# Kernel tuning notes

Hardware: AMD Instinct MI355X
Metric: run time of the kernel (lower is better)

Reference implementation:

```python
import jax, jax.numpy as jnp
import numpy as np

N_NODES = 4096
N_EDGES = 131072
IN_DIM = 40
HID = 128
OUT = 128
GAT_H = 2
GAT_C = 64
D_MODEL = 128
N_HEAD = 4
FF_DIM = 2048
N_LAYERS = 2
EPS = 1e-5
NEG_SLOPE = 0.2


def _layer_norm(x, g, b):
    mu = x.mean(-1, keepdims=True)
    var = ((x - mu) ** 2).mean(-1, keepdims=True)
    return (x - mu) / jnp.sqrt(var + EPS) * g + b


def _gat_conv(h, src, dst, W, a_src, a_dst, bias):
    # PyG GATConv, concat=True, eval mode (no dropout). Self loops already in (src, dst).
    N = h.shape[0]
    xw = (h @ W.T).reshape(N, GAT_H, GAT_C)          # [N, H, C]
    al_src = (xw * a_src).sum(-1)                     # [N, H]
    al_dst = (xw * a_dst).sum(-1)                     # [N, H]
    e = jax.nn.leaky_relu(al_src[src] + al_dst[dst], NEG_SLOPE)  # [E, H]
    # segment softmax over incoming edges of each dst node
    m = jax.ops.segment_max(e, dst, num_segments=N)
    ex = jnp.exp(e - m[dst])
    s = jax.ops.segment_sum(ex, dst, num_segments=N)
    alpha = ex / (s[dst] + 1e-16)                     # [E, H]
    out = jax.ops.segment_sum(xw[src] * alpha[..., None], dst, num_segments=N)
    return out.reshape(N, GAT_H * GAT_C) + bias


def _encoder_layer(x, p):
    # post-norm nn.TransformerEncoderLayer, relu FFN, eval mode
    (in_w, in_b, out_w, out_b, ln1_g, ln1_b,
     ff_w1, ff_b1, ff_w2, ff_b2, ln2_g, ln2_b) = p
    S, E = x.shape
    Dh = E // N_HEAD
    qkv = x @ in_w.T + in_b                           # [S, 3E]
    q, k, v = [t.reshape(S, N_HEAD, Dh) for t in jnp.split(qkv, 3, axis=-1)]
    scores = jnp.einsum('shd,thd->hst', q, k) / jnp.asarray(np.sqrt(Dh), x.dtype)
    attn = jax.nn.softmax(scores, axis=-1)            # [H, S, S]
    o = jnp.einsum('hst,thd->shd', attn, v).reshape(S, E) @ out_w.T + out_b
    x = _layer_norm(x + o, ln1_g, ln1_b)
    ff = jax.nn.relu(x @ ff_w1.T + ff_b1) @ ff_w2.T + ff_b2
    return _layer_norm(x + ff, ln2_g, ln2_b)


def _forward(floats, edge_index):
    (x, enc_w1, enc_b1, enc_w2, enc_b2,
     gat_w, gat_asrc, gat_adst, gat_b,
     l0_in_w, l0_in_b, l0_out_w, l0_out_b, l0_ln1_g, l0_ln1_b,
     l0_ff_w1, l0_ff_b1, l0_ff_w2, l0_ff_b2, l0_ln2_g, l0_ln2_b,
     l1_in_w, l1_in_b, l1_out_w, l1_out_b, l1_ln1_g, l1_ln1_b,
     l1_ff_w1, l1_ff_b1, l1_ff_w2, l1_ff_b2, l1_ln2_g, l1_ln2_b) = floats
    N = x.shape[0]
    # encoder MLP
    h = jax.nn.relu(x @ enc_w1.T + enc_b1) @ enc_w2.T + enc_b2
    # add one self loop per node (GATConv add_self_loops semantics)
    loop = jnp.arange(N, dtype=edge_index.dtype)
    src = jnp.concatenate([edge_index[0], loop])
    dst = jnp.concatenate([edge_index[1], loop])
    h = _gat_conv(h, src, dst, gat_w, gat_asrc, gat_adst, gat_b)
    layers = [
        (l0_in_w, l0_in_b, l0_out_w, l0_out_b, l0_ln1_g, l0_ln1_b,
         l0_ff_w1, l0_ff_b1, l0_ff_w2, l0_ff_b2, l0_ln2_g, l0_ln2_b),
        (l1_in_w, l1_in_b, l1_out_w, l1_out_b, l1_ln1_g, l1_ln1_b,
         l1_ff_w1, l1_ff_b1, l1_ff_w2, l1_ff_b2, l1_ln2_g, l1_ln2_b),
    ]
    for p in layers:
        h = _encoder_layer(h, p)
    return h


def setup_inputs() -> dict:
    key = jax.random.key(0)
    ks = jax.random.split(key, 40)
    s = 0.05
    inp = {}
    inp['x'] = jax.random.normal(ks[0], (N_NODES, IN_DIM), dtype=jnp.float32)
    # edges with src != dst (self loops added inside reference)
    src = jax.random.randint(ks[1], (N_EDGES,), 0, N_NODES)
    off = jax.random.randint(ks[2], (N_EDGES,), 1, N_NODES)
    dst = (src + off) % N_NODES
    inp['edge_index'] = jnp.stack([src, dst]).astype(jnp.int64)
    inp['enc_w1'] = jax.random.normal(ks[3], (HID, IN_DIM)) * s
    inp['enc_b1'] = jnp.zeros((HID,), jnp.float32)
    inp['enc_w2'] = jax.random.normal(ks[4], (OUT, HID)) * s
    inp['enc_b2'] = jnp.zeros((OUT,), jnp.float32)
    inp['gat_w'] = jax.random.normal(ks[5], (GAT_H * GAT_C, OUT)) * s
    inp['gat_asrc'] = jax.random.normal(ks[6], (GAT_H, GAT_C)) * s
    inp['gat_adst'] = jax.random.normal(ks[7], (GAT_H, GAT_C)) * s
    inp['gat_b'] = jnp.zeros((GAT_H * GAT_C,), jnp.float32)
    for i in range(N_LAYERS):
        k = jax.random.split(ks[8 + i], 8)
        inp[f'l{i}_in_w'] = jax.random.normal(k[0], (3 * D_MODEL, D_MODEL)) * s
        inp[f'l{i}_in_b'] = jnp.zeros((3 * D_MODEL,), jnp.float32)
        inp[f'l{i}_out_w'] = jax.random.normal(k[1], (D_MODEL, D_MODEL)) * s
        inp[f'l{i}_out_b'] = jnp.zeros((D_MODEL,), jnp.float32)
        inp[f'l{i}_ln1_g'] = jnp.ones((D_MODEL,), jnp.float32)
        inp[f'l{i}_ln1_b'] = jnp.zeros((D_MODEL,), jnp.float32)
        inp[f'l{i}_ff_w1'] = jax.random.normal(k[2], (FF_DIM, D_MODEL)) * s
        inp[f'l{i}_ff_b1'] = jnp.zeros((FF_DIM,), jnp.float32)
        inp[f'l{i}_ff_w2'] = jax.random.normal(k[3], (D_MODEL, FF_DIM)) * s
        inp[f'l{i}_ff_b2'] = jnp.zeros((D_MODEL,), jnp.float32)
        inp[f'l{i}_ln2_g'] = jnp.ones((D_MODEL,), jnp.float32)
        inp[f'l{i}_ln2_b'] = jnp.zeros((D_MODEL,), jnp.float32)
    return inp


def reference(x, edge_index, enc_w1, enc_b1, enc_w2, enc_b2,
              gat_w, gat_asrc, gat_adst, gat_b,
              l0_in_w, l0_in_b, l0_out_w, l0_out_b, l0_ln1_g, l0_ln1_b,
              l0_ff_w1, l0_ff_b1, l0_ff_w2, l0_ff_b2, l0_ln2_g, l0_ln2_b,
              l1_in_w, l1_in_b, l1_out_w, l1_out_b, l1_ln1_g, l1_ln1_b,
              l1_ff_w1, l1_ff_b1, l1_ff_w2, l1_ff_b2, l1_ln2_g, l1_ln2_b):
    floats = (x, enc_w1, enc_b1, enc_w2, enc_b2,
              gat_w, gat_asrc, gat_adst, gat_b,
              l0_in_w, l0_in_b, l0_out_w, l0_out_b, l0_ln1_g, l0_ln1_b,
              l0_ff_w1, l0_ff_b1, l0_ff_w2, l0_ff_b2, l0_ln2_g, l0_ln2_b,
              l1_in_w, l1_in_b, l1_out_w, l1_out_b, l1_ln1_g, l1_ln1_b,
              l1_ff_w1, l1_ff_b1, l1_ff_w2, l1_ff_b2, l1_ln2_g, l1_ln2_b)
    return _forward(floats, edge_index)
```

## Files before the change

kernel.cpp:

```cpp
#include <hip/hip_runtime.h>
#include <hip/hip_bf16.h>

typedef __hip_bfloat16 bf16;

#define N_NODES 4096
#define IN_DIM  40
#define DM      128
#define FF_DIM  2048
#define GAT_H   2
#define GAT_C   64
#define NHEAD   4
#define DH      32
#define LN_EPS  1e-5f
#define KSPLIT  4
#define FSPLIT  4

typedef short s8v __attribute__((ext_vector_type(8)));
typedef float f4v __attribute__((ext_vector_type(4)));

#define WO_ENC1 0
#define WO_ENC2 8192
#define WO_GAT  24576
#define WO_L(L) (40960 + (L) * 589824)
#define WO_IN(L)  (WO_L(L))
#define WO_OUT(L) (WO_L(L) + 49152)
#define WO_FF1(L) (WO_L(L) + 65536)
#define WO_FF2(L) (WO_L(L) + 327680)
#define WBUF_ELEMS 1220608

__device__ __forceinline__ float anyload(const void* p, size_t i, int isbf) {
    if (isbf) return __bfloat162float(((const bf16*)p)[i]);
    return ((const float*)p)[i];
}
__device__ __forceinline__ int geti(const int* ei, int i, int is64) {
    return is64 ? ei[2 * (size_t)i] : ei[i];
}
__device__ __forceinline__ ushort tob(float v) {
    bf16 b = __float2bfloat16(v);
    return *(ushort*)&b;
}

__global__ __launch_bounds__(256) void setup_kernel(const void* ones_vec, const int* ei,
                                                    int* flags, int* __restrict__ deg,
                                                    const void* enc_w1, const void* enc_w2,
                                                    const void* gat_w,
                                                    const void* in_w0, const void* out_w0,
                                                    const void* ff_w10, const void* ff_w20,
                                                    const void* in_w1, const void* out_w1,
                                                    const void* ff_w11, const void* ff_w21,
                                                    ushort* __restrict__ wbuf) {
    const int isbf = (((const unsigned*)ones_vec)[0] == 0x3F803F80u) ? 1 : 0;
    int gid = blockIdx.x * 256 + threadIdx.x;
    if (gid < N_NODES) deg[gid] = 0;
    if (gid == 0) {
        flags[0] = isbf;
        const unsigned* e = (const unsigned*)ei;
        flags[1] = (e[1] == 0u && e[3] == 0u && e[5] == 0u && e[7] == 0u) ? 1 : 0;
    }
    int base = gid * 4;
#pragma unroll
    for (int j = 0; j < 4; ++j) {
        int i = base + j;
        if (i >= WBUF_ELEMS) break;
        if (i < WO_ENC2) {
            int r = i >> 6, c = i & 63;
            float v = (c < IN_DIM) ? anyload(enc_w1, (size_t)r * IN_DIM + c, isbf) : 0.f;
            wbuf[i] = tob(v);
            continue;
        }
        const void* s;
        int si;
        if      (i < WO_GAT)     { s = enc_w2; si = i - WO_ENC2; }
        else if (i < WO_L(0))    { s = gat_w;  si = i - WO_GAT; }
        else if (i < WO_OUT(0))  { s = in_w0;  si = i - WO_IN(0); }
        else if (i < WO_FF1(0))  { s = out_w0; si = i - WO_OUT(0); }
        else if (i < WO_FF2(0))  { s = ff_w10; si = i - WO_FF1(0); }
        else if (i < WO_L(1))    { s = ff_w20; si = i - WO_FF2(0); }
        else if (i < WO_OUT(1))  { s = in_w1;  si = i - WO_IN(1); }
        else if (i < WO_FF1(1))  { s = out_w1; si = i - WO_OUT(1); }
        else if (i < WO_FF2(1))  { s = ff_w11; si = i - WO_FF1(1); }
        else                     { s = ff_w21; si = i - WO_FF2(1); }
        wbuf[i] = isbf ? ((const ushort*)s)[si] : tob(((const float*)s)[si]);
    }
}

#define K128STR 136

__global__ __launch_bounds__(256) void encgat_kernel(const void* __restrict__ X,
                                                     const void* __restrict__ b1v,
                                                     const void* __restrict__ b2v,
// ... 97 lines not shown
#pragma unroll
    for (int nc = 0; nc < 2; ++nc) {
        int cc = w * 32 + nc * 16 + col;
#pragma unroll
        for (int r = 0; r < 4; ++r) {
            int row = quad * 4 + r;
            float v = acc3[nc][r];
            xwout[(size_t)(row0 + row) * DM + cc] = v;
            Cs[row][cc] = v;
        }
    }
    __syncthreads();
#pragma unroll
    for (int rr = 0; rr < 4; ++rr) {
        int row = w * 4 + rr;
        float x0 = Cs[row][lane], x1 = Cs[row][64 + lane];
        float s0 = x0 * anyload(asrc, lane, isbf);
        float d0 = x0 * anyload(adst, lane, isbf);
        float s1 = x1 * anyload(asrc, 64 + lane, isbf);
        float d1 = x1 * anyload(adst, 64 + lane, isbf);
#pragma unroll
        for (int o = 32; o >= 1; o >>= 1) {
            s0 += __shfl_xor(s0, o); d0 += __shfl_xor(d0, o);
            s1 += __shfl_xor(s1, o); d1 += __shfl_xor(d1, o);
        }
        if (lane == 0) {
            int n = row0 + row;
            als[n * 2 + 0] = s0; ald[n * 2 + 0] = d0;
            als[n * 2 + 1] = s1; ald[n * 2 + 1] = d1;
        }
    }
}

__global__ __launch_bounds__(256) void gemm32_kernel(const ushort* __restrict__ A,
                                                     const ushort* __restrict__ Wb,
                                                     const void* __restrict__ bias,
                                                     ushort* __restrict__ Cb,
                                                     ushort* __restrict__ vtb,
                                                     int N,
                                                     const int* __restrict__ flags,
                                                     int relu) {
    const int isbf = flags[0];
    const int t = threadIdx.x;
    const int w = t >> 6, lane = t & 63;
    const int col = lane & 15, quad = lane >> 4;
    const int wr = (w & 1) * 16, wc = (w >> 1) * 32;
    const int row0 = blockIdx.y * 32, col0 = blockIdx.x * 64;
    __shared__ __align__(16) ushort As[32 * K128STR];
    __shared__ __align__(16) ushort Ws[64 * K128STR];
#pragma unroll
    for (int i = 0; i < 2; ++i) {
        int idx = t + i * 256;
        int r = idx >> 4, c = (idx & 15) * 8;
        *(uint4*)&As[r * K128STR + c] = *(const uint4*)&A[(size_t)(row0 + r) * DM + c];
    }
#pragma unroll
    for (int i = 0; i < 4; ++i) {
        int idx = t + i * 256;
        int r = idx >> 4, c = (idx & 15) * 8;
        *(uint4*)&Ws[r * K128STR + c] = *(const uint4*)&Wb[(size_t)(col0 + r) * DM + c];
    }
    __syncthreads();
    f4v zero = {0.f, 0.f, 0.f, 0.f};
    f4v acc[2] = {zero, zero};
#pragma unroll
    for (int j = 0; j < 4; ++j) {
        s8v a = *(const s8v*)&As[(wr + col) * K128STR + j * 32 + quad * 8];
#pragma unroll
        for (int nc = 0; nc < 2; ++nc) {
            s8v b = *(const s8v*)&Ws[(wc + nc * 16 + col) * K128STR + j * 32 + quad * 8];
            acc[nc] = __builtin_amdgcn_mfma_f32_16x16x32_bf16(a, b, acc[nc], 0, 0, 0);
        }
    }
#pragma unroll
    for (int nc = 0; nc < 2; ++nc) {
        int cc = col0 + wc + nc * 16 + col;
        float bv = bias ? anyload(bias, cc, isbf) : 0.f;
#pragma unroll
        for (int r = 0; r < 4; ++r) {
            int rr = row0 + wr + quad * 4 + r;
            float v = acc[nc][r] + bv;
            if (relu) v = fmaxf(v, 0.f);
            Cb[(size_t)rr * N + cc] = tob(v);
            if (vtb && cc >= 256) vtb[(size_t)(cc - 256) * N_NODES + rr] = tob(v);
        }
    }
}

__global__ __launch_bounds__(256) void oproj_ln_kernel(const float* __restrict__ pO,
                                                       const float* __restrict__ pL,
                                                       const ushort* __restrict__ Wb,
                                                       const void* __restrict__ bias,
                                                       float* __restrict__ h,
                                                       ushort* __restrict__ hb,
                                                       const void* __restrict__ g,
                                                       const void* __restrict__ b,
                                                       const int* __restrict__ flags) {
    const int isbf = flags[0];
    const int t = threadIdx.x;
    const int w = t >> 6, lane = t & 63;
    const int col = lane & 15, quad = lane >> 4;
    const int row0 = blockIdx.x * 16;
    __shared__ __align__(16) ushort As[16 * K128STR];
    __shared__ __align__(16) ushort Ws[128 * K128STR];
    __shared__ float Cs[16][132];

    {
        int ar = t >> 4, ac = (t & 15) * 8;
        int rr = row0 + ar;
        int hh = ac >> 5, d0 = ac & 31;
        size_t qi0 = ((size_t)rr) * NHEAD + hh;
        float lsum = 0.f;
        float osum[8] = {};
#pragma unroll
        for (int kz = 0; kz < KSPLIT; ++kz) {
            size_t qi = qi0 + (size_t)kz * N_NODES * NHEAD;
            lsum += pL[qi];
            const float* po = &pO[qi * 32 + d0];
#pragma unroll
            for (int j = 0; j < 8; ++j) osum[j] += po[j];
        }
        float inv = 1.f / lsum;
#pragma unroll
        for (int j = 0; j < 8; ++j) As[ar * K128STR + ac + j] = tob(osum[j] * inv);
    }
#pragma unroll
    for (int i = 0; i < 8; ++i) {
        int idx = t + i * 256;
        int r = idx >> 4, c = (idx & 15) * 8;
        *(uint4*)&Ws[r * K128STR + c] = *(const uint4*)&Wb[(size_t)r * DM + c];
    }
    __syncthreads();
    f4v zero = {0.f, 0.f, 0.f, 0.f};
    f4v acc[2] = {zero, zero};
#pragma unroll
    for (int j = 0; j < 4; ++j) {
        s8v a = *(const s8v*)&As[col * K128STR + j * 32 + quad * 8];
#pragma unroll
        for (int nc = 0; nc < 2; ++nc) {
            s8v b = *(const s8v*)&Ws[(w * 32 + nc * 16 + col) * K128STR + j * 32 + quad * 8];
            acc[nc] = __builtin_amdgcn_mfma_f32_16x16x32_bf16(a, b, acc[nc], 0, 0, 0);
        }
    }
#pragma unroll
    for (int nc = 0; nc < 2; ++nc) {
        int cc = w * 32 + nc * 16 + col;
        float bv = bias ? anyload(bias, cc, isbf) : 0.f;
#pragma unroll
        for (int r = 0; r < 4; ++r)
            Cs[quad * 4 + r][cc] = acc[nc][r] + bv;
    }
    __syncthreads();
#pragma unroll
    for (int rr = 0; rr < 4; ++rr) {
        int row = w * 4 + rr;
        size_t base = (size_t)(row0 + row) * DM;
        float v0 = h[base + lane] + Cs[row][lane];
        float v1 = h[base + 64 + lane] + Cs[row][64 + lane];
        float s = v0 + v1;
#pragma unroll
        for (int o = 32; o >= 1; o >>= 1) s += __shfl_xor(s, o);
        float mu = s * (1.f / DM);
        float d0 = v0 - mu, d1 = v1 - mu;
        float q = d0 * d0 + d1 * d1;
#pragma unroll
        for (int o = 32; o >= 1; o >>= 1) q += __shfl_xor(q, o);
        float rstd = rsqrtf(q * (1.f / DM) + LN_EPS);
        float o0 = d0 * rstd * anyload(g, lane, isbf) + anyload(b, lane, isbf);
        float o1 = d1 * rstd * anyload(g, 64 + lane, isbf) + anyload(b, 64 + lane, isbf);
        h[base + lane] = o0;       h[base + 64 + lane] = o1;
        hb[base + lane] = tob(o0); hb[base + 64 + lane] = tob(o1);
    }
}

__global__ __launch_bounds__(256) void ff2_splitk_kernel(const ushort* __restrict__ A,
                                                         const ushort* __restrict__ Wb,
                                                         float* __restrict__ Cpart) {
    const int t = threadIdx.x;
    const int w = t >> 6, lane = t & 63;
    const int col = lane & 15, quad = lane >> 4;
    const int row0 = blockIdx.x * 64;
    const int ks = blockIdx.y;
    const int k_beg = ks * (FF_DIM / FSPLIT);
    __shared__ __align__(16) ushort As[64 * K128STR];
    __shared__ __align__(16) ushort Ws[128 * K128STR];
    f4v zero = {0.f, 0.f, 0.f, 0.f};
    f4v acc[8] = {zero, zero, zero, zero, zero, zero, zero, zero};
    const int wr = w * 16;

    for (int it = 0; it < 4; ++it) {
        int k0 = k_beg + it * 128;
        __syncthreads();
#pragma unroll
        for (int i = 0; i < 4; ++i) {
            int idx = t + i * 256;
            int r = idx >> 4, c = (idx & 15) * 8;
            *(uint4*)&As[r * K128STR + c] = *(const uint4*)&A[(size_t)(row0 + r) * FF_DIM + k0 + c];
        }
#pragma unroll
        for (int i = 0; i < 8; ++i) {
            int idx = t + i * 256;
            int r = idx >> 4, c = (idx & 15) * 8;
            *(uint4*)&Ws[r * K128STR + c] = *(const uint4*)&Wb[(size_t)r * FF_DIM + k0 + c];
        }
        __syncthreads();
#pragma unroll
        for (int j = 0; j < 4; ++j) {
            s8v a = *(const s8v*)&As[(wr + col) * K128STR + j * 32 + quad * 8];
#pragma unroll
            for (int nc = 0; nc < 8; ++nc) {
                s8v b = *(const s8v*)&Ws[(nc * 16 + col) * K128STR + j * 32 + quad * 8];
                acc[nc] = __builtin_amdgcn_mfma_f32_16x16x32_bf16(a, b, acc[nc], 0, 0, 0);
            }
        }
    }
#pragma unroll
    for (int nc = 0; nc < 8; ++nc) {
        int cc = nc * 16 + col;
#pragma unroll
        for (int r = 0; r < 4; ++r) {
            int rr = row0 + wr + quad * 4 + r;
            Cpart[((size_t)ks * N_NODES + rr) * DM + cc] = acc[nc][r];
        }
    }
}

__global__ __launch_bounds__(256) void ln4_kernel(float* __restrict__ h,
                                                  const float* __restrict__ pC,
                                                  const void* __restrict__ fbias,
                                                  ushort* __restrict__ hb,
                                                  const void* __restrict__ g, const void* __restrict__ b,
                                                  void* __restrict__ outp,
                                                  const int* __restrict__ flags) {
    const int isbf = flags[0];
    const int row = blockIdx.x * 4 + (threadIdx.x >> 6);
    const int lane = threadIdx.x & 63;
    const size_t base = (size_t)row * DM;
    float y0 = anyload(fbias, lane, isbf), y1 = anyload(fbias, 64 + lane, isbf);
#pragma unroll
    for (int kz = 0; kz < FSPLIT; ++kz) {
        size_t pb = (size_t)kz * N_NODES * DM + base;
        y0 += pC[pb + lane];
        y1 += pC[pb + 64 + lane];
    }
    float v0 = h[base + lane] + y0;
    float v1 = h[base + 64 + lane] + y1;
    float s = v0 + v1;
#pragma unroll
    for (int o = 32; o >= 1; o >>= 1) s += __shfl_xor(s, o);
    float mu = s * (1.f / DM);
    float d0 = v0 - mu, d1 = v1 - mu;
    float q = d0 * d0 + d1 * d1;
#pragma unroll
    for (int o = 32; o >= 1; o >>= 1) q += __shfl_xor(q, o);
    float rstd = rsqrtf(q * (1.f / DM) + LN_EPS);
    float o0 = d0 * rstd * anyload(g, lane, isbf) + anyload(b, lane, isbf);
    float o1 = d1 * rstd * anyload(g, 64 + lane, isbf) + anyload(b, 64 + lane, isbf);
    h[base + lane] = o0;       h[base + 64 + lane] = o1;
    hb[base + lane] = tob(o0); hb[base + 64 + lane] = tob(o1);
    if (outp) {
        if (isbf) {
            ((ushort*)outp)[base + lane] = tob(o0);
            ((ushort*)outp)[base + 64 + lane] = tob(o1);
        } else {
            ((float*)outp)[base + lane] = o0;
            ((float*)outp)[base + 64 + lane] = o1;
        }
    }
}

__global__ void deg_hist_kernel(const int* __restrict__ ei, int E0,
                                int* __restrict__ deg, const int* __restrict__ flags) {
    const int is64 = flags[1];
    int e = blockIdx.x * 256 + threadIdx.x;
    int E = E0 + N_NODES;
    if (e >= E) return;
    int d = (e < E0) ? geti(ei, E0 + e, is64) : (e - E0);
    atomicAdd(&deg[d], 1);
}

__global__ __launch_bounds__(256) void scan_kernel(const int* __restrict__ deg,
                                                   int* __restrict__ rowptr,
                                                   int* __restrict__ cursor) {
    __shared__ int part[256];
    const int t = threadIdx.x;
    const int base = t * 16;
    int loc[16];
    int s = 0;
#pragma unroll
    for (int i = 0; i < 16; ++i) { loc[i] = s; s += deg[base + i]; }
    part[t] = s;
    __syncthreads();
    for (int d = 1; d < 256; d <<= 1) {
        int v = (t >= d) ? part[t - d] : 0;
        __syncthreads();
        part[t] += v;
        __syncthreads();
    }
    int prev = (t == 0) ? 0 : part[t - 1];
#pragma unroll
    for (int i = 0; i < 16; ++i) {
        int r = prev + loc[i];
        rowptr[base + i] = r;
// ... 38 lines not shown
        v = (v > 0.f) ? v : 0.2f * v;
        mx = fmaxf(mx, v);
    }
#pragma unroll
    for (int o = 32; o >= 1; o >>= 1) mx = fmaxf(mx, __shfl_xor(mx, o));
    float sm = 0.f;
    for (int i = beg + lane; i < end; i += 64) {
        int s = csr_src[i];
        float v = als[s * 2 + hh] + aldv;
        v = (v > 0.f) ? v : 0.2f * v;
        sm += __expf(v - mx);
    }
#pragma unroll
    for (int o = 32; o >= 1; o >>= 1) sm += __shfl_xor(sm, o);
    const float inv = 1.f / (sm + 1e-16f);

    float o_acc = 0.f;
    for (int i = beg; i < end; ++i) {
        int s = csr_src[i];
        float v = als[s * 2 + hh] + aldv;
        v = (v > 0.f) ? v : 0.2f * v;
        float alpha = __expf(v - mx) * inv;
        o_acc += alpha * xw[(size_t)s * DM + hh * GAT_C + lane];
    }
    float outv = o_acc + anyload(gat_b, hh * GAT_C + lane, isbf);
    size_t off = (size_t)d * DM + hh * GAT_C + lane;
    hg[off] = outv;
    hgb[off] = tob(outv);
}

#define KSTR 40
#define VSTR 136
#define PSTR 136
__global__ __launch_bounds__(256) void attn_mfma_kernel(const ushort* __restrict__ qkvb,
                                                        const ushort* __restrict__ vtb,
                                                        float* __restrict__ pO,
                                                        float* __restrict__ pL) {
    const int hh = blockIdx.y;
    const int kz = blockIdx.z;
    const int t = threadIdx.x;
    const int w = t >> 6;
    const int lane = t & 63;
    const int col = lane & 15;
    const int quad = lane >> 4;
    const int qr = blockIdx.x * 64 + w * 16;

    __shared__ __align__(16) ushort Ks[128 * KSTR];
    __shared__ __align__(16) ushort Vt[32 * VSTR];
    __shared__ __align__(16) ushort Pl[4][16 * PSTR];

    s8v aq = *(const s8v*)&qkvb[(size_t)(qr + col) * 384 + hh * 32 + quad * 8];

    f4v zero = {0.f, 0.f, 0.f, 0.f};
    f4v of[2] = {zero, zero};
    float lacc[4] = {0.f, 0.f, 0.f, 0.f};
    const float scale = 0.17677669529663687f;
    const int k_beg = kz * (N_NODES / KSPLIT);
    const int k_end = k_beg + (N_NODES / KSPLIT);

    for (int kt = k_beg; kt < k_end; kt += 128) {
        __syncthreads();
        for (int idx = t; idx < 512; idx += 256) {
            int r = idx >> 2, c = (idx & 3) * 8;
            *(uint4*)&Ks[r * KSTR + c] =
                *(const uint4*)&qkvb[(size_t)(kt + r) * 384 + 128 + hh * 32 + c];
        }
        for (int idx = t; idx < 512; idx += 256) {
            int d = idx >> 4, c = (idx & 15) * 8;
            *(uint4*)&Vt[d * VSTR + c] =
                *(const uint4*)&vtb[(size_t)(hh * 32 + d) * N_NODES + kt + c];
        }
        __syncthreads();

        f4v sf[8];
#pragma unroll
        for (int kb = 0; kb < 8; ++kb) {
            s8v bk = *(const s8v*)&Ks[(kb * 16 + col) * KSTR + quad * 8];
            sf[kb] = __builtin_amdgcn_mfma_f32_16x16x32_bf16(aq, bk, zero, 0, 0, 0);
        }
#pragma unroll
        for (int kb = 0; kb < 8; ++kb) {
#pragma unroll
            for (int r = 0; r < 4; ++r) {
                float p = __expf(sf[kb][r] * scale);
                lacc[r] += p;
                Pl[w][(quad * 4 + r) * PSTR + kb * 16 + col] = tob(p);
            }
        }
#pragma unroll
        for (int kc = 0; kc < 4; ++kc) {
            s8v ap = *(const s8v*)&Pl[w][col * PSTR + kc * 32 + quad * 8];
#pragma unroll
            for (int nc = 0; nc < 2; ++nc) {
                s8v bv = *(const s8v*)&Vt[(nc * 16 + col) * VSTR + kc * 32 + quad * 8];
                of[nc] = __builtin_amdgcn_mfma_f32_16x16x32_bf16(ap, bv, of[nc], 0, 0, 0);
            }
        }
    }
#pragma unroll
    for (int r = 0; r < 4; ++r) {
        float lv = lacc[r];
#pragma unroll
        for (int off = 1; off <= 8; off <<= 1) lv += __shfl_xor(lv, off);
        int row = quad * 4 + r;
        size_t qi = ((size_t)kz * N_NODES + qr + row) * NHEAD + hh;
#pragma unroll
        for (int nc = 0; nc < 2; ++nc)
            pO[qi * 32 + nc * 16 + col] = of[nc][r];
        if (col == 0) pL[qi] = lv;
    }
}

extern "C" void kernel_launch(void* const* d_in, const int* in_sizes, int n_in,
                              void* d_out, int out_size, void* d_ws, size_t ws_size,
                              hipStream_t stream) {
    const void* x        = d_in[0];
    const int*  ei       = (const int*)d_in[1];
    const void* enc_w1   = d_in[2];
    const void* enc_b1   = d_in[3];
    const void* enc_w2   = d_in[4];
    const void* enc_b2   = d_in[5];
    const void* gat_w    = d_in[6];
    const void* gat_asrc = d_in[7];
    const void* gat_adst = d_in[8];
    const void* gat_b    = d_in[9];
    const void *in_w[2], *in_b[2], *out_w[2], *out_b[2], *ln1_g[2], *ln1_b[2];
    const void *ff_w1[2], *ff_b1[2], *ff_w2[2], *ff_b2[2], *ln2_g[2], *ln2_b[2];
    for (int L = 0; L < 2; ++L) {
        int base = 10 + L * 12;
        in_w[L]  = d_in[base + 0];
        in_b[L]  = d_in[base + 1];
        out_w[L] = d_in[base + 2];
        out_b[L] = d_in[base + 3];
        ln1_g[L] = d_in[base + 4];
        ln1_b[L] = d_in[base + 5];
        ff_w1[L] = d_in[base + 6];
        ff_b1[L] = d_in[base + 7];
        ff_w2[L] = d_in[base + 8];
        ff_b2[L] = d_in[base + 9];
        ln2_g[L] = d_in[base + 10];
        ln2_b[L] = d_in[base + 11];
    }
    const int E0 = in_sizes[1] / 2;
    const int E  = E0 + N_NODES;
    const size_t NN = N_NODES;

    int*    flags   = (int*)d_ws;
    float*  h       = (float*)d_ws + 64;
    ushort* hb      = (ushort*)(h + NN * DM);
    ushort* qkvb    = hb + NN * DM;
    ushort* vtb     = qkvb + NN * 384;
    ushort* ff1b    = vtb + NN * DM;
    ushort* wbuf    = ff1b + NN * FF_DIM;
    float*  pO      = (float*)(wbuf + WBUF_ELEMS);
    float*  pL      = pO + (size_t)KSPLIT * NN * NHEAD * 32;
    float*  pC      = pL + (size_t)KSPLIT * NN * NHEAD;
    float*  xw      = pC + (size_t)FSPLIT * NN * DM;
    float*  als     = xw + NN * DM;
    float*  ald     = als + NN * GAT_H;
    int*    deg     = (int*)(ald + NN * GAT_H);
    int*    rowptr  = deg + N_NODES;
    int*    cursor  = rowptr + N_NODES + 1;
    int*    csr_src = cursor + N_NODES;

    dim3 blk(256);

    setup_kernel<<<dim3((WBUF_ELEMS + 1023) / 1024), blk, 0, stream>>>(
        ln1_g[0], ei, flags, deg,
        enc_w1, enc_w2, gat_w, in_w[0], out_w[0], ff_w1[0], ff_w2[0],
        in_w[1], out_w[1], ff_w1[1], ff_w2[1], wbuf);
    deg_hist_kernel<<<dim3((E + 255) / 256), blk, 0, stream>>>(ei, E0, deg, flags);
    scan_kernel<<<dim3(1), blk, 0, stream>>>(deg, rowptr, cursor);
    scatter_kernel<<<dim3((E + 255) / 256), blk, 0, stream>>>(ei, E0, cursor, csr_src, flags);

    encgat_kernel<<<dim3(N_NODES / 16), blk, 0, stream>>>(
        x, enc_b1, enc_b2, wbuf, gat_asrc, gat_adst, xw, als, ald, flags);
    gat_gather_kernel<<<dim3(N_NODES * GAT_H / 4), blk, 0, stream>>>(
        rowptr, csr_src, als, ald, xw, gat_b, h, hb, flags);

    for (int L = 0; L < 2; ++L) {
        gemm32_kernel<<<dim3(3 * DM / 64, N_NODES / 32), blk, 0, stream>>>(
            hb, wbuf + WO_IN(L), in_b[L], qkvb, vtb, 3 * DM, flags, 0);
        attn_mfma_kernel<<<dim3(N_NODES / 64, NHEAD, KSPLIT), blk, 0, stream>>>(
            qkvb, vtb, pO, pL);
        oproj_ln_kernel<<<dim3(N_NODES / 16), blk, 0, stream>>>(
            pO, pL, wbuf + WO_OUT(L), out_b[L], h, hb, ln1_g[L], ln1_b[L], flags);
        gemm32_kernel<<<dim3(FF_DIM / 64, N_NODES / 32), blk, 0, stream>>>(
            hb, wbuf + WO_FF1(L), ff_b1[L], ff1b, nullptr, FF_DIM, flags, 1);
        ff2_splitk_kernel<<<dim3(N_NODES / 64, FSPLIT), blk, 0, stream>>>(
            ff1b, wbuf + WO_FF2(L), pC);
        ln4_kernel<<<dim3(N_NODES / 4), blk, 0, stream>>>(
            h, pC, ff_b2[L], hb, ln2_g[L], ln2_b[L],
            (L == 1) ? d_out : nullptr, flags);
    }
}
```

Measured before the change: 318.1 us.

## Fuse transformer layer stages into one persistent kernel with grid barriers

Replaces the six per-layer kernel launches (QKV GEMM, attention, out-proj+LN, FF1, FF2 split-K, LN) with one persistent kernel of 512 blocks that loops over tiles for each stage and separates the stages with a software grid barrier built on global atomics. The goal is to remove launch overhead and inter-kernel gaps. In exchange every stage is now limited to 512 resident blocks with a shared LDS buffer, and the kernel depends on all blocks being co-resident for the spin barrier to make progress. The barrier adds atomic round-trips at each stage boundary.

Measured after the change: 926.0 us. +191.1%, slower.

```diff
diff --git a/kernel.cpp b/kernel.cpp
--- a/kernel.cpp
+++ b/kernel.cpp
@@ -14,6 +14,7 @@
 #define LN_EPS  1e-5f
 #define KSPLIT  4
 #define FSPLIT  4
+#define GRID    512
 
 typedef short s8v __attribute__((ext_vector_type(8)));
 typedef float f4v __attribute__((ext_vector_type(4)));
@@ -38,6 +39,24 @@
 __device__ __forceinline__ ushort tob(float v) {
     bf16 b = __float2bfloat16(v);
     return *(ushort*)&b;
+}
+
+__device__ __forceinline__ void gridbar(int* bar) {
+    __syncthreads();
+    if (threadIdx.x == 0) {
+        int g = __hip_atomic_load(&bar[1], __ATOMIC_RELAXED, __HIP_MEMORY_SCOPE_AGENT);
+        __threadfence();
+        int a = __hip_atomic_fetch_add(&bar[0], 1, __ATOMIC_RELAXED, __HIP_MEMORY_SCOPE_AGENT);
+        if (a == GRID - 1) {
+            __hip_atomic_store(&bar[0], 0, __ATOMIC_RELAXED, __HIP_MEMORY_SCOPE_AGENT);
+            __hip_atomic_store(&bar[1], g + 1, __ATOMIC_RELEASE, __HIP_MEMORY_SCOPE_AGENT);
+        } else {
+            while (__hip_atomic_load(&bar[1], __ATOMIC_RELAXED, __HIP_MEMORY_SCOPE_AGENT) == g)
+                __builtin_amdgcn_s_sleep(2);
+        }
+        __threadfence();
+    }
+    __syncthreads();
 }
 
 __global__ __launch_bounds__(256) void setup_kernel(const void* ones_vec, const int* ei,
@@ -56,6 +75,8 @@
         flags[0] = isbf;
         const unsigned* e = (const unsigned*)ei;
         flags[1] = (e[1] == 0u && e[3] == 0u && e[5] == 0u && e[7] == 0u) ? 1 : 0;
+        flags[8] = 0;
+        flags[9] = 0;
     }
     int base = gid * 4;
 #pragma unroll
@@ -219,243 +240,6 @@
     }
 }
 
-__global__ __launch_bounds__(256) void gemm32_kernel(const ushort* __restrict__ A,
-                                                     const ushort* __restrict__ Wb,
-                                                     const void* __restrict__ bias,
-                                                     ushort* __restrict__ Cb,
-                                                     ushort* __restrict__ vtb,
-                                                     int N,
-                                                     const int* __restrict__ flags,
-                                                     int relu) {
-    const int isbf = flags[0];
-    const int t = threadIdx.x;
-    const int w = t >> 6, lane = t & 63;
-    const int col = lane & 15, quad = lane >> 4;
-    const int wr = (w & 1) * 16, wc = (w >> 1) * 32;
-    const int row0 = blockIdx.y * 32, col0 = blockIdx.x * 64;
-    __shared__ __align__(16) ushort As[32 * K128STR];
-    __shared__ __align__(16) ushort Ws[64 * K128STR];
-#pragma unroll
-    for (int i = 0; i < 2; ++i) {
-        int idx = t + i * 256;
-        int r = idx >> 4, c = (idx & 15) * 8;
-        *(uint4*)&As[r * K128STR + c] = *(const uint4*)&A[(size_t)(row0 + r) * DM + c];
-    }
-#pragma unroll
-    for (int i = 0; i < 4; ++i) {
-        int idx = t + i * 256;
-        int r = idx >> 4, c = (idx & 15) * 8;
-        *(uint4*)&Ws[r * K128STR + c] = *(const uint4*)&Wb[(size_t)(col0 + r) * DM + c];
-    }
-    __syncthreads();
-    f4v zero = {0.f, 0.f, 0.f, 0.f};
-    f4v acc[2] = {zero, zero};
-#pragma unroll
-    for (int j = 0; j < 4; ++j) {
-        s8v a = *(const s8v*)&As[(wr + col) * K128STR + j * 32 + quad * 8];
-#pragma unroll
-        for (int nc = 0; nc < 2; ++nc) {
-            s8v b = *(const s8v*)&Ws[(wc + nc * 16 + col) * K128STR + j * 32 + quad * 8];
-            acc[nc] = __builtin_amdgcn_mfma_f32_16x16x32_bf16(a, b, acc[nc], 0, 0, 0);
-        }
-    }
-#pragma unroll
-    for (int nc = 0; nc < 2; ++nc) {
-        int cc = col0 + wc + nc * 16 + col;
-        float bv = bias ? anyload(bias, cc, isbf) : 0.f;
-#pragma unroll
-        for (int r = 0; r < 4; ++r) {
-            int rr = row0 + wr + quad * 4 + r;
-            float v = acc[nc][r] + bv;
-            if (relu) v = fmaxf(v, 0.f);
-            Cb[(size_t)rr * N + cc] = tob(v);
-            if (vtb && cc >= 256) vtb[(size_t)(cc - 256) * N_NODES + rr] = tob(v);
-        }
-    }
-}
-
-__global__ __launch_bounds__(256) void oproj_ln_kernel(const float* __restrict__ pO,
-                                                       const float* __restrict__ pL,
-                                                       const ushort* __restrict__ Wb,
-                                                       const void* __restrict__ bias,
-                                                       float* __restrict__ h,
-                                                       ushort* __restrict__ hb,
-                                                       const void* __restrict__ g,
-                                                       const void* __restrict__ b,
-                                                       const int* __restrict__ flags) {
-    const int isbf = flags[0];
-    const int t = threadIdx.x;
-    const int w = t >> 6, lane = t & 63;
-    const int col = lane & 15, quad = lane >> 4;
-    const int row0 = blockIdx.x * 16;
-    __shared__ __align__(16) ushort As[16 * K128STR];
-    __shared__ __align__(16) ushort Ws[128 * K128STR];
-    __shared__ float Cs[16][132];
-
-    {
-        int ar = t >> 4, ac = (t & 15) * 8;
-        int rr = row0 + ar;
-        int hh = ac >> 5, d0 = ac & 31;
-        size_t qi0 = ((size_t)rr) * NHEAD + hh;
-        float lsum = 0.f;
-        float osum[8] = {};
-#pragma unroll
-        for (int kz = 0; kz < KSPLIT; ++kz) {
-            size_t qi = qi0 + (size_t)kz * N_NODES * NHEAD;
-            lsum += pL[qi];
-            const float* po = &pO[qi * 32 + d0];
-#pragma unroll
-            for (int j = 0; j < 8; ++j) osum[j] += po[j];
-        }
-        float inv = 1.f / lsum;
-#pragma unroll
-        for (int j = 0; j < 8; ++j) As[ar * K128STR + ac + j] = tob(osum[j] * inv);
-    }
-#pragma unroll
-    for (int i = 0; i < 8; ++i) {
-        int idx = t + i * 256;
-        int r = idx >> 4, c = (idx & 15) * 8;
-        *(uint4*)&Ws[r * K128STR + c] = *(const uint4*)&Wb[(size_t)r * DM + c];
-    }
-    __syncthreads();
-    f4v zero = {0.f, 0.f, 0.f, 0.f};
-    f4v acc[2] = {zero, zero};
-#pragma unroll
-    for (int j = 0; j < 4; ++j) {
-        s8v a = *(const s8v*)&As[col * K128STR + j * 32 + quad * 8];
-#pragma unroll
-        for (int nc = 0; nc < 2; ++nc) {
-            s8v b = *(const s8v*)&Ws[(w * 32 + nc * 16 + col) * K128STR + j * 32 + quad * 8];
-            acc[nc] = __builtin_amdgcn_mfma_f32_16x16x32_bf16(a, b, acc[nc], 0, 0, 0);
-        }
-    }
-#pragma unroll
-    for (int nc = 0; nc < 2; ++nc) {
-        int cc = w * 32 + nc * 16 + col;
-        float bv = bias ? anyload(bias, cc, isbf) : 0.f;
-#pragma unroll
-        for (int r = 0; r < 4; ++r)
-            Cs[quad * 4 + r][cc] = acc[nc][r] + bv;
-    }
-    __syncthreads();
-#pragma unroll
-    for (int rr = 0; rr < 4; ++rr) {
-        int row = w * 4 + rr;
-        size_t base = (size_t)(row0 + row) * DM;
-        float v0 = h[base + lane] + Cs[row][lane];
-        float v1 = h[base + 64 + lane] + Cs[row][64 + lane];
-        float s = v0 + v1;
-#pragma unroll
-        for (int o = 32; o >= 1; o >>= 1) s += __shfl_xor(s, o);
-        float mu = s * (1.f / DM);
-        float d0 = v0 - mu, d1 = v1 - mu;
-        float q = d0 * d0 + d1 * d1;
-#pragma unroll
-        for (int o = 32; o >= 1; o >>= 1) q += __shfl_xor(q, o);
-        float rstd = rsqrtf(q * (1.f / DM) + LN_EPS);
-        float o0 = d0 * rstd * anyload(g, lane, isbf) + anyload(b, lane, isbf);
-        float o1 = d1 * rstd * anyload(g, 64 + lane, isbf) + anyload(b, 64 + lane, isbf);
-        h[base + lane] = o0;       h[base + 64 + lane] = o1;
-        hb[base + lane] = tob(o0); hb[base + 64 + lane] = tob(o1);
-    }
-}
-
-__global__ __launch_bounds__(256) void ff2_splitk_kernel(const ushort* __restrict__ A,
-                                                         const ushort* __restrict__ Wb,
-                                                         float* __restrict__ Cpart) {
-    const int t = threadIdx.x;
-    const int w = t >> 6, lane = t & 63;
-    const int col = lane & 15, quad = lane >> 4;
-    const int row0 = blockIdx.x * 64;
-    const int ks = blockIdx.y;
-    const int k_beg = ks * (FF_DIM / FSPLIT);
-    __shared__ __align__(16) ushort As[64 * K128STR];
-    __shared__ __align__(16) ushort Ws[128 * K128STR];
-    f4v zero = {0.f, 0.f, 0.f, 0.f};
-    f4v acc[8] = {zero, zero, zero, zero, zero, zero, zero, zero};
-    const int wr = w * 16;
-
-    for (int it = 0; it < 4; ++it) {
-        int k0 = k_beg + it * 128;
-        __syncthreads();
-#pragma unroll
-        for (int i = 0; i < 4; ++i) {
-            int idx = t + i * 256;
-            int r = idx >> 4, c = (idx & 15) * 8;
-            *(uint4*)&As[r * K128STR + c] = *(const uint4*)&A[(size_t)(row0 + r) * FF_DIM + k0 + c];
-        }
-#pragma unroll
-        for (int i = 0; i < 8; ++i) {
-            int idx = t + i * 256;
-            int r = idx >> 4, c = (idx & 15) * 8;
-            *(uint4*)&Ws[r * K128STR + c] = *(const uint4*)&Wb[(size_t)r * FF_DIM + k0 + c];
-        }
-        __syncthreads();
-#pragma unroll
-        for (int j = 0; j < 4; ++j) {
-            s8v a = *(const s8v*)&As[(wr + col) * K128STR + j * 32 + quad * 8];
-#pragma unroll
-            for (int nc = 0; nc < 8; ++nc) {
-                s8v b = *(const s8v*)&Ws[(nc * 16 + col) * K128STR + j * 32 + quad * 8];
-                acc[nc] = __builtin_amdgcn_mfma_f32_16x16x32_bf16(a, b, acc[nc], 0, 0, 0);
-            }
-        }
-    }
-#pragma unroll
-    for (int nc = 0; nc < 8; ++nc) {
-        int cc = nc * 16 + col;
-#pragma unroll
-        for (int r = 0; r < 4; ++r) {
-            int rr = row0 + wr + quad * 4 + r;
-            Cpart[((size_t)ks * N_NODES + rr) * DM + cc] = acc[nc][r];
-        }
-    }
-}
-
-__global__ __launch_bounds__(256) void ln4_kernel(float* __restrict__ h,
-                                                  const float* __restrict__ pC,
-                                                  const void* __restrict__ fbias,
-                                                  ushort* __restrict__ hb,
-                                                  const void* __restrict__ g, const void* __restrict__ b,
-                                                  void* __restrict__ outp,
-                                                  const int* __restrict__ flags) {
-    const int isbf = flags[0];
-    const int row = blockIdx.x * 4 + (threadIdx.x >> 6);
-    const int lane = threadIdx.x & 63;
-    const size_t base = (size_t)row * DM;
-    float y0 = anyload(fbias, lane, isbf), y1 = anyload(fbias, 64 + lane, isbf);
-#pragma unroll
-    for (int kz = 0; kz < FSPLIT; ++kz) {
-        size_t pb = (size_t)kz * N_NODES * DM + base;
-        y0 += pC[pb + lane];
-        y1 += pC[pb + 64 + lane];
-    }
-    float v0 = h[base + lane] + y0;
-    float v1 = h[base + 64 + lane] + y1;
-    float s = v0 + v1;
-#pragma unroll
-    for (int o = 32; o >= 1; o >>= 1) s += __shfl_xor(s, o);
-    float mu = s * (1.f / DM);
-    float d0 = v0 - mu, d1 = v1 - mu;
-    float q = d0 * d0 + d1 * d1;
-#pragma unroll
-    for (int o = 32; o >= 1; o >>= 1) q += __shfl_xor(q, o);
-    float rstd = rsqrtf(q * (1.f / DM) + LN_EPS);
-    float o0 = d0 * rstd * anyload(g, lane, isbf) + anyload(b, lane, isbf);
-    float o1 = d1 * rstd * anyload(g, 64 + lane, isbf) + anyload(b, 64 + lane, isbf);
-    h[base + lane] = o0;       h[base + 64 + lane] = o1;
-    hb[base + lane] = tob(o0); hb[base + 64 + lane] = tob(o1);
-    if (outp) {
-        if (isbf) {
-            ((ushort*)outp)[base + lane] = tob(o0);
-            ((ushort*)outp)[base + 64 + lane] = tob(o1);
-        } else {
-            ((float*)outp)[base + lane] = o0;
-            ((float*)outp)[base + 64 + lane] = o1;
-        }
-    }
-}
-
 __global__ void deg_hist_kernel(const int* __restrict__ ei, int E0,
                                 int* __restrict__ deg, const int* __restrict__ flags) {
     const int is64 = flags[1];
@@ -560,82 +344,348 @@
 #define KSTR 40
 #define VSTR 136
 #define PSTR 136
-__global__ __launch_bounds__(256) void attn_mfma_kernel(const ushort* __restrict__ qkvb,
-                                                        const ushort* __restrict__ vtb,
-                                                        float* __restrict__ pO,
-                                                        float* __restrict__ pL) {
-    const int hh = blockIdx.y;
-    const int kz = blockIdx.z;
+#define SH_USHORTS 26112
+
+__global__ __launch_bounds__(256, 2) void layer_kernel(
+        const ushort* __restrict__ w_in, const ushort* __restrict__ w_out,
+        const ushort* __restrict__ w_ff1, const ushort* __restrict__ w_ff2,
+        const void* __restrict__ in_b, const void* __restrict__ out_b,
+        const void* __restrict__ ln1_g, const void* __restrict__ ln1_b,
+        const void* __restrict__ ff_b1, const void* __restrict__ ff_b2,
+        const void* __restrict__ ln2_g, const void* __restrict__ ln2_b,
+        float* __restrict__ h, ushort* __restrict__ hb,
+        ushort* __restrict__ qkvb, ushort* __restrict__ vtb,
+        float* __restrict__ pO, float* __restrict__ pL,
+        float* __restrict__ pC, ushort* __restrict__ ff1b,
+        void* __restrict__ outp, const int* __restrict__ flags, int* __restrict__ bar) {
+    const int isbf = flags[0];
     const int t = threadIdx.x;
-    const int w = t >> 6;
-    const int lane = t & 63;
-    const int col = lane & 15;
-    const int quad = lane >> 4;
-    const int qr = blockIdx.x * 64 + w * 16;
-
-    __shared__ __align__(16) ushort Ks[128 * KSTR];
-    __shared__ __align__(16) ushort Vt[32 * VSTR];
-    __shared__ __align__(16) ushort Pl[4][16 * PSTR];
-
-    s8v aq = *(const s8v*)&qkvb[(size_t)(qr + col) * 384 + hh * 32 + quad * 8];
-
+    const int w = t >> 6, lane = t & 63;
+    const int col = lane & 15, quad = lane >> 4;
+    __shared__ __align__(16) ushort SH[SH_USHORTS];
     f4v zero = {0.f, 0.f, 0.f, 0.f};
-    f4v of[2] = {zero, zero};
-    float lacc[4] = {0.f, 0.f, 0.f, 0.f};
-    const float scale = 0.17677669529663687f;
-    const int k_beg = kz * (N_NODES / KSPLIT);
-    const int k_end = k_beg + (N_NODES / KSPLIT);
-
-    for (int kt = k_beg; kt < k_end; kt += 128) {
-        __syncthreads();
-        for (int idx = t; idx < 512; idx += 256) {
-            int r = idx >> 2, c = (idx & 3) * 8;
-            *(uint4*)&Ks[r * KSTR + c] =
-                *(const uint4*)&qkvb[(size_t)(kt + r) * 384 + 128 + hh * 32 + c];
-        }
-        for (int idx = t; idx < 512; idx += 256) {
-            int d = idx >> 4, c = (idx & 15) * 8;
-            *(uint4*)&Vt[d * VSTR + c] =
-                *(const uint4*)&vtb[(size_t)(hh * 32 + d) * N_NODES + kt + c];
-        }
-        __syncthreads();
-
-        f4v sf[8];
-#pragma unroll
-        for (int kb = 0; kb < 8; ++kb) {
-            s8v bk = *(const s8v*)&Ks[(kb * 16 + col) * KSTR + quad * 8];
-            sf[kb] = __builtin_amdgcn_mfma_f32_16x16x32_bf16(aq, bk, zero, 0, 0, 0);
-        }
-#pragma unroll
-        for (int kb = 0; kb < 8; ++kb) {
+
+    {
+        ushort* As = SH;
+        ushort* Ws = SH + 32 * K128STR;
+        const int wr = (w & 1) * 16, wc = (w >> 1) * 32;
+        for (int tile = blockIdx.x; tile < 768; tile += GRID) {
+            int colt = tile % 6, rowt = tile / 6;
+            int row0 = rowt * 32, col0 = colt * 64;
+            __syncthreads();
+#pragma unroll
+            for (int i = 0; i < 2; ++i) {
+                int idx = t + i * 256;
+                int r = idx >> 4, c = (idx & 15) * 8;
+                *(uint4*)&As[r * K128STR + c] = *(const uint4*)&hb[(size_t)(row0 + r) * DM + c];
+            }
+#pragma unroll
+            for (int i = 0; i < 4; ++i) {
+                int idx = t + i * 256;
+                int r = idx >> 4, c = (idx & 15) * 8;
+                *(uint4*)&Ws[r * K128STR + c] = *(const uint4*)&w_in[(size_t)(col0 + r) * DM + c];
+            }
+            __syncthreads();
+            f4v acc[2] = {zero, zero};
+#pragma unroll
+            for (int j = 0; j < 4; ++j) {
+                s8v a = *(const s8v*)&As[(wr + col) * K128STR + j * 32 + quad * 8];
+#pragma unroll
+                for (int nc = 0; nc < 2; ++nc) {
+                    s8v b = *(const s8v*)&Ws[(wc + nc * 16 + col) * K128STR + j * 32 + quad * 8];
+                    acc[nc] = __builtin_amdgcn_mfma_f32_16x16x32_bf16(a, b, acc[nc], 0, 0, 0);
+                }
+            }
+#pragma unroll
+            for (int nc = 0; nc < 2; ++nc) {
+                int cc = col0 + wc + nc * 16 + col;
+                float bv = anyload(in_b, cc, isbf);
+#pragma unroll
+                for (int r = 0; r < 4; ++r) {
+                    int rr = row0 + wr + quad * 4 + r;
+                    ushort hv = tob(acc[nc][r] + bv);
+                    qkvb[(size_t)rr * 384 + cc] = hv;
+                    if (cc >= 256) vtb[(size_t)(cc - 256) * N_NODES + rr] = hv;
+                }
+            }
+        }
+    }
+    gridbar(bar);
+
+    {
+        ushort* Ks = SH;
+        ushort* Vt = SH + 128 * KSTR;
+        ushort* Pw = SH + 128 * KSTR + 32 * VSTR + w * 16 * PSTR;
+        const float scale = 0.17677669529663687f;
+        for (int tile = blockIdx.x; tile < 1024; tile += GRID) {
+            int qx = tile & 63, hh = (tile >> 6) & 3, kz = tile >> 8;
+            int qr = qx * 64 + w * 16;
+            s8v aq = *(const s8v*)&qkvb[(size_t)(qr + col) * 384 + hh * 32 + quad * 8];
+            f4v of[2] = {zero, zero};
+            float lacc[4] = {0.f, 0.f, 0.f, 0.f};
+            const int k_beg = kz * (N_NODES / KSPLIT);
+            const int k_end = k_beg + (N_NODES / KSPLIT);
+            for (int kt = k_beg; kt < k_end; kt += 128) {
+                __syncthreads();
+                for (int idx = t; idx < 512; idx += 256) {
+                    int r = idx >> 2, c = (idx & 3) * 8;
+                    *(uint4*)&Ks[r * KSTR + c] =
+                        *(const uint4*)&qkvb[(size_t)(kt + r) * 384 + 128 + hh * 32 + c];
+                }
+                for (int idx = t; idx < 512; idx += 256) {
+                    int d = idx >> 4, c = (idx & 15) * 8;
+                    *(uint4*)&Vt[d * VSTR + c] =
+                        *(const uint4*)&vtb[(size_t)(hh * 32 + d) * N_NODES + kt + c];
+                }
+                __syncthreads();
+                f4v sf[8];
+#pragma unroll
+                for (int kb = 0; kb < 8; ++kb) {
+                    s8v bk = *(const s8v*)&Ks[(kb * 16 + col) * KSTR + quad * 8];
+                    sf[kb] = __builtin_amdgcn_mfma_f32_16x16x32_bf16(aq, bk, zero, 0, 0, 0);
+                }
+#pragma unroll
+                for (int kb = 0; kb < 8; ++kb) {
+#pragma unroll
+                    for (int r = 0; r < 4; ++r) {
+                        float p = __expf(sf[kb][r] * scale);
+                        lacc[r] += p;
+                        Pw[(quad * 4 + r) * PSTR + kb * 16 + col] = tob(p);
+                    }
+                }
+#pragma unroll
+                for (int kc = 0; kc < 4; ++kc) {
+                    s8v ap = *(const s8v*)&Pw[col * PSTR + kc * 32 + quad * 8];
+#pragma unroll
+                    for (int nc = 0; nc < 2; ++nc) {
+                        s8v bv = *(const s8v*)&Vt[(nc * 16 + col) * VSTR + kc * 32 + quad * 8];
+                        of[nc] = __builtin_amdgcn_mfma_f32_16x16x32_bf16(ap, bv, of[nc], 0, 0, 0);
+                    }
+                }
+            }
 #pragma unroll
             for (int r = 0; r < 4; ++r) {
-                float p = __expf(sf[kb][r] * scale);
-                lacc[r] += p;
-                Pl[w][(quad * 4 + r) * PSTR + kb * 16 + col] = tob(p);
-            }
-        }
-#pragma unroll
-        for (int kc = 0; kc < 4; ++kc) {
-            s8v ap = *(const s8v*)&Pl[w][col * PSTR + kc * 32 + quad * 8];
+                float lv = lacc[r];
+#pragma unroll
+                for (int off = 1; off <= 8; off <<= 1) lv += __shfl_xor(lv, off);
+                int row = quad * 4 + r;
+                size_t qi = ((size_t)kz * N_NODES + qr + row) * NHEAD + hh;
+#pragma unroll
+                for (int nc = 0; nc < 2; ++nc)
+                    pO[qi * 32 + nc * 16 + col] = of[nc][r];
+                if (col == 0) pL[qi] = lv;
+            }
+        }
+    }
+    gridbar(bar);
+
+    {
+        ushort* As = SH;
+        ushort* Ws = SH + 16 * K128STR;
+        float*  Cs = (float*)(SH + 16 * K128STR + 128 * K128STR);
+        for (int tile = blockIdx.x; tile < 256; tile += GRID) {
+            int row0 = tile * 16;
+            __syncthreads();
+            {
+                int ar = t >> 4, ac = (t & 15) * 8;
+                int rr = row0 + ar;
+                int hh = ac >> 5, d0 = ac & 31;
+                size_t qi0 = ((size_t)rr) * NHEAD + hh;
+                float lsum = 0.f;
+                float osum[8] = {};
+#pragma unroll
+                for (int kz = 0; kz < KSPLIT; ++kz) {
+                    size_t qi = qi0 + (size_t)kz * N_NODES * NHEAD;
+                    lsum += pL[qi];
+                    const float* po = &pO[qi * 32 + d0];
+#pragma unroll
+                    for (int j = 0; j < 8; ++j) osum[j] += po[j];
+                }
+                float inv = 1.f / lsum;
+#pragma unroll
+                for (int j = 0; j < 8; ++j) As[ar * K128STR + ac + j] = tob(osum[j] * inv);
+            }
+#pragma unroll
+            for (int i = 0; i < 8; ++i) {
+                int idx = t + i * 256;
+                int r = idx >> 4, c = (idx & 15) * 8;
+                *(uint4*)&Ws[r * K128STR + c] = *(const uint4*)&w_out[(size_t)r * DM + c];
+            }
+            __syncthreads();
+            f4v acc[2] = {zero, zero};
+#pragma unroll
+            for (int j = 0; j < 4; ++j) {
+                s8v a = *(const s8v*)&As[col * K128STR + j * 32 + quad * 8];
+#pragma unroll
+                for (int nc = 0; nc < 2; ++nc) {
+                    s8v b = *(const s8v*)&Ws[(w * 32 + nc * 16 + col) * K128STR + j * 32 + quad * 8];
+                    acc[nc] = __builtin_amdgcn_mfma_f32_16x16x32_bf16(a, b, acc[nc], 0, 0, 0);
+                }
+            }
 #pragma unroll
             for (int nc = 0; nc < 2; ++nc) {
-                s8v bv = *(const s8v*)&Vt[(nc * 16 + col) * VSTR + kc * 32 + quad * 8];
-                of[nc] = __builtin_amdgcn_mfma_f32_16x16x32_bf16(ap, bv, of[nc], 0, 0, 0);
-            }
-        }
-    }
-#pragma unroll
-    for (int r = 0; r < 4; ++r) {
-        float lv = lacc[r];
-#pragma unroll
-        for (int off = 1; off <= 8; off <<= 1) lv += __shfl_xor(lv, off);
-        int row = quad * 4 + r;
-        size_t qi = ((size_t)kz * N_NODES + qr + row) * NHEAD + hh;
-#pragma unroll
-        for (int nc = 0; nc < 2; ++nc)
-            pO[qi * 32 + nc * 16 + col] = of[nc][r];
-        if (col == 0) pL[qi] = lv;
+                int cc = w * 32 + nc * 16 + col;
+                float bv = anyload(out_b, cc, isbf);
+#pragma unroll
+                for (int r = 0; r < 4; ++r)
+                    Cs[(quad * 4 + r) * 132 + cc] = acc[nc][r] + bv;
+            }
+            __syncthreads();
+#pragma unroll
+            for (int rr = 0; rr < 4; ++rr) {
+                int row = w * 4 + rr;
+                size_t base = (size_t)(row0 + row) * DM;
+                float v0 = h[base + lane] + Cs[row * 132 + lane];
+                float v1 = h[base + 64 + lane] + Cs[row * 132 + 64 + lane];
+                float s = v0 + v1;
+#pragma unroll
+                for (int o = 32; o >= 1; o >>= 1) s += __shfl_xor(s, o);
+                float mu = s * (1.f / DM);
+                float d0 = v0 - mu, d1 = v1 - mu;
+                float q = d0 * d0 + d1 * d1;
+#pragma unroll
+                for (int o = 32; o >= 1; o >>= 1) q += __shfl_xor(q, o);
+                float rstd = rsqrtf(q * (1.f / DM) + LN_EPS);
+                float o0 = d0 * rstd * anyload(ln1_g, lane, isbf) + anyload(ln1_b, lane, isbf);
+                float o1 = d1 * rstd * anyload(ln1_g, 64 + lane, isbf) + anyload(ln1_b, 64 + lane, isbf);
+                h[base + lane] = o0;       h[base + 64 + lane] = o1;
+                hb[base + lane] = tob(o0); hb[base + 64 + lane] = tob(o1);
+            }
+        }
+    }
+    gridbar(bar);
+
+    {
+        ushort* As = SH;
+        ushort* Ws = SH + 64 * K128STR;
+        const int wr = w * 16;
+        for (int tile = blockIdx.x; tile < 1024; tile += GRID) {
+            int rowt = tile & 63, colt = tile >> 6;
+            int row0 = rowt * 64, colb = colt * 128;
+            __syncthreads();
+#pragma unroll
+            for (int i = 0; i < 4; ++i) {
+                int idx = t + i * 256;
+                int r = idx >> 4, c = (idx & 15) * 8;
+                *(uint4*)&As[r * K128STR + c] = *(const uint4*)&hb[(size_t)(row0 + r) * DM + c];
+            }
+#pragma unroll
+            for (int i = 0; i < 8; ++i) {
+                int idx = t + i * 256;
+                int r = idx >> 4, c = (idx & 15) * 8;
+                *(uint4*)&Ws[r * K128STR + c] = *(const uint4*)&w_ff1[(size_t)(colb + r) * DM + c];
+            }
+            __syncthreads();
+            f4v acc[8] = {zero, zero, zero, zero, zero, zero, zero, zero};
+#pragma unroll
+            for (int j = 0; j < 4; ++j) {
+                s8v a = *(const s8v*)&As[(wr + col) * K128STR + j * 32 + quad * 8];
+#pragma unroll
+                for (int nc = 0; nc < 8; ++nc) {
+                    s8v b = *(const s8v*)&Ws[(nc * 16 + col) * K128STR + j * 32 + quad * 8];
+                    acc[nc] = __builtin_amdgcn_mfma_f32_16x16x32_bf16(a, b, acc[nc], 0, 0, 0);
+                }
+            }
+#pragma unroll
+            for (int nc = 0; nc < 8; ++nc) {
+                int cc = colb + nc * 16 + col;
+                float bv = anyload(ff_b1, cc, isbf);
+#pragma unroll
+                for (int r = 0; r < 4; ++r) {
+                    int rr = row0 + wr + quad * 4 + r;
+                    ff1b[(size_t)rr * FF_DIM + cc] = tob(fmaxf(acc[nc][r] + bv, 0.f));
+                }
+            }
+        }
+    }
+    gridbar(bar);
+
+    {
+        ushort* As = SH;
+        ushort* Ws = SH + 64 * K128STR;
+        const int wr = w * 16;
+        for (int tile = blockIdx.x; tile < 64 * FSPLIT; tile += GRID) {
+            int rowt = tile & 63, ks = tile >> 6;
+            int row0 = rowt * 64;
+            int k_beg = ks * (FF_DIM / FSPLIT);
+            f4v acc[8] = {zero, zero, zero, zero, zero, zero, zero, zero};
+            for (int it = 0; it < 4; ++it) {
+                int k0 = k_beg + it * 128;
+                __syncthreads();
+#pragma unroll
+                for (int i = 0; i < 4; ++i) {
+                    int idx = t + i * 256;
+                    int r = idx >> 4, c = (idx & 15) * 8;
+                    *(uint4*)&As[r * K128STR + c] =
+                        *(const uint4*)&ff1b[(size_t)(row0 + r) * FF_DIM + k0 + c];
+                }
+#pragma unroll
+                for (int i = 0; i < 8; ++i) {
+                    int idx = t + i * 256;
+                    int r = idx >> 4, c = (idx & 15) * 8;
+                    *(uint4*)&Ws[r * K128STR + c] =
+                        *(const uint4*)&w_ff2[(size_t)r * FF_DIM + k0 + c];
+                }
+                __syncthreads();
+#pragma unroll
+                for (int j = 0; j < 4; ++j) {
+                    s8v a = *(const s8v*)&As[(wr + col) * K128STR + j * 32 + quad * 8];
+#pragma unroll
+                    for (int nc = 0; nc < 8; ++nc) {
+                        s8v b = *(const s8v*)&Ws[(nc * 16 + col) * K128STR + j * 32 + quad * 8];
+                        acc[nc] = __builtin_amdgcn_mfma_f32_16x16x32_bf16(a, b, acc[nc], 0, 0, 0);
+                    }
+                }
+            }
+#pragma unroll
+            for (int nc = 0; nc < 8; ++nc) {
+                int cc = nc * 16 + col;
+#pragma unroll
+                for (int r = 0; r < 4; ++r) {
+                    int rr = row0 + wr + quad * 4 + r;
+                    pC[((size_t)ks * N_NODES + rr) * DM + cc] = acc[nc][r];
+                }
+            }
+        }
+    }
+    gridbar(bar);
+
+    {
+        for (int tile = blockIdx.x; tile < 1024; tile += GRID) {
+            int row = tile * 4 + (t >> 6);
+            size_t base = (size_t)row * DM;
+            float y0 = anyload(ff_b2, lane, isbf), y1 = anyload(ff_b2, 64 + lane, isbf);
+#pragma unroll
+            for (int kz = 0; kz < FSPLIT; ++kz) {
+                size_t pb = (size_t)kz * N_NODES * DM + base;
+                y0 += pC[pb + lane];
+                y1 += pC[pb + 64 + lane];
+            }
+            float v0 = h[base + lane] + y0;
+            float v1 = h[base + 64 + lane] + y1;
+            float s = v0 + v1;
+#pragma unroll
+            for (int o = 32; o >= 1; o >>= 1) s += __shfl_xor(s, o);
+            float mu = s * (1.f / DM);
+            float d0 = v0 - mu, d1 = v1 - mu;
+            float q = d0 * d0 + d1 * d1;
+#pragma unroll
+            for (int o = 32; o >= 1; o >>= 1) q += __shfl_xor(q, o);
+            float rstd = rsqrtf(q * (1.f / DM) + LN_EPS);
+            float o0 = d0 * rstd * anyload(ln2_g, lane, isbf) + anyload(ln2_b, lane, isbf);
+            float o1 = d1 * rstd * anyload(ln2_g, 64 + lane, isbf) + anyload(ln2_b, 64 + lane, isbf);
+            h[base + lane] = o0;       h[base + 64 + lane] = o1;
+            hb[base + lane] = tob(o0); hb[base + 64 + lane] = tob(o1);
+            if (outp) {
+                if (isbf) {
+                    ((ushort*)outp)[base + lane] = tob(o0);
+                    ((ushort*)outp)[base + 64 + lane] = tob(o1);
+                } else {
+                    ((float*)outp)[base + lane] = o0;
+                    ((float*)outp)[base + 64 + lane] = o1;
+                }
+            }
+        }
     }
 }
 
@@ -690,6 +740,7 @@
     int*    rowptr  = deg + N_NODES;
     int*    cursor  = rowptr + N_NODES + 1;
     int*    csr_src = cursor + N_NODES;
+    int*    bar     = flags + 8;
 
     dim3 blk(256);
 
@@ -707,18 +758,10 @@
         rowptr, csr_src, als, ald, xw, gat_b, h, hb, flags);
 
     for (int L = 0; L < 2; ++L) {
-        gemm32_kernel<<<dim3(3 * DM / 64, N_NODES / 32), blk, 0, stream>>>(
-            hb, wbuf + WO_IN(L), in_b[L], qkvb, vtb, 3 * DM, flags, 0);
-        attn_mfma_kernel<<<dim3(N_NODES / 64, NHEAD, KSPLIT), blk, 0, stream>>>(
-            qkvb, vtb, pO, pL);
-        oproj_ln_kernel<<<dim3(N_NODES / 16), blk, 0, stream>>>(
-            pO, pL, wbuf + WO_OUT(L), out_b[L], h, hb, ln1_g[L], ln1_b[L], flags);
-        gemm32_kernel<<<dim3(FF_DIM / 64, N_NODES / 32), blk, 0, stream>>>(
-            hb, wbuf + WO_FF1(L), ff_b1[L], ff1b, nullptr, FF_DIM, flags, 1);
-        ff2_splitk_kernel<<<dim3(N_NODES / 64, FSPLIT), blk, 0, stream>>>(
-            ff1b, wbuf + WO_FF2(L), pC);
-        ln4_kernel<<<dim3(N_NODES / 4), blk, 0, stream>>>(
-            h, pC, ff_b2[L], hb, ln2_g[L], ln2_b[L],
-            (L == 1) ? d_out : nullptr, flags);
-    }
-}
+        layer_kernel<<<dim3(GRID), blk, 0, stream>>>(
+            wbuf + WO_IN(L), wbuf + WO_OUT(L), wbuf + WO_FF1(L), wbuf + WO_FF2(L),
+            in_b[L], out_b[L], ln1_g[L], ln1_b[L], ff_b1[L], ff_b2[L], ln2_g[L], ln2_b[L],
+            h, hb, qkvb, vtb, pO, pL, pC, ff1b,
+            (L == 1) ? d_out : nullptr, flags, bar);
+    }
+}
```
